# Optimization experiments

Hardware: AMD Instinct MI355X
Metric: run time of the kernel (lower is better)

## Reference

```python
import jax, jax.numpy as jnp
import numpy as np

SEQ_LEN = 32768
HID = 1024


def setup_inputs() -> dict:
    key = jax.random.key(0)
    k1, k2, k3, k4 = jax.random.split(key, 4)
    hidden = jax.random.normal(k1, (1, 1, HID), dtype=jnp.float32)
    encoder_outputs = jax.random.normal(k2, (SEQ_LEN, HID), dtype=jnp.float32)
    # nn.Linear(hidden_size, hidden_size): weight [H, H], bias [H]
    W = jax.random.normal(k3, (HID, HID), dtype=jnp.float32) * (1.0 / np.sqrt(HID))
    b = jax.random.normal(k4, (HID,), dtype=jnp.float32) * 0.01
    return {"hidden": hidden, "encoder_outputs": encoder_outputs, "W": W, "b": b}


def reference(hidden, encoder_outputs, W, b):
    # method == 'general':
    #   energy_i = Linear(enc_i) = W @ enc_i + b     -> [S, H]
    #   e_i = sum(hidden[-1, 0] * energy_i)           -> [S]
    h = hidden[-1, 0]                                 # [H]
    proj = jnp.einsum('sh,dh->sd', encoder_outputs, W) + b  # [S, H]
    energies = proj @ h                               # [S]
    attn = jax.nn.softmax(energies, axis=0)           # [S]
    return attn[None, None, :]                        # [1, 1, S]
```

## Files before the change

kernel.cpp:

```cpp
#include <hip/hip_runtime.h>
#include <hip/hip_bf16.h>
#include <math.h>

#define SEQ_LEN 32768
#define HID 1024

__global__ void __launch_bounds__(256) k_matvec(const float* __restrict__ W,
                                                const float* __restrict__ hvec,
                                                float* __restrict__ v) {
    __shared__ float red[256];
    const int t = threadIdx.x;
    const int col = (blockIdx.x << 5) + (t & 31);
    const int slice = t >> 5;
    const int d0 = slice << 7;
    float acc = 0.f;
#pragma unroll 8
    for (int dd = 0; dd < 128; ++dd) {
        const int d = d0 + dd;
        acc += hvec[d] * W[d * HID + col];
    }
    red[t] = acc;
    __syncthreads();
    if (t < 32) {
        float s = 0.f;
#pragma unroll
        for (int i = 0; i < 8; ++i) s += red[(i << 5) + t];
        v[(blockIdx.x << 5) + t] = s;
    }
}

__global__ void __launch_bounds__(256) k_energy(const float* __restrict__ enc,
                                                const float* __restrict__ v,
                                                float* __restrict__ energies,
                                                float2* __restrict__ bstats) {
    const int t = threadIdx.x;
    const int wave = t >> 6;
    const int lane = t & 63;
    const int row0 = (blockIdx.x << 5) + (wave << 3);

    const float4 vr0 = *reinterpret_cast<const float4*>(v +       (lane << 2));
    const float4 vr1 = *reinterpret_cast<const float4*>(v + 256 + (lane << 2));
    const float4 vr2 = *reinterpret_cast<const float4*>(v + 512 + (lane << 2));
    const float4 vr3 = *reinterpret_cast<const float4*>(v + 768 + (lane << 2));

    float m = -__builtin_inff();
    float z = 0.f;

#pragma unroll 2
    for (int r = 0; r < 8; ++r) {
        const size_t row = (size_t)(row0 + r);
        const float4* p = reinterpret_cast<const float4*>(enc + row * HID) + lane;
        const float4 a = p[0];
        const float4 b = p[64];
        const float4 c = p[128];
        const float4 d = p[192];
        float acc = a.x * vr0.x + a.y * vr0.y + a.z * vr0.z + a.w * vr0.w
                  + b.x * vr1.x + b.y * vr1.y + b.z * vr1.z + b.w * vr1.w
                  + c.x * vr2.x + c.y * vr2.y + c.z * vr2.z + c.w * vr2.w
                  + d.x * vr3.x + d.y * vr3.y + d.z * vr3.z + d.w * vr3.w;
#pragma unroll
        for (int off = 32; off; off >>= 1) acc += __shfl_xor(acc, off, 64);
        if (lane == 0) energies[row] = acc;
        const float nm = fmaxf(m, acc);
        z = z * __expf(m - nm) + __expf(acc - nm);
        m = nm;
    }

    __shared__ float wm[4], wz[4];
    if (lane == 0) { wm[wave] = m; wz[wave] = z; }
    __syncthreads();
    if (t == 0) {
        float M = fmaxf(fmaxf(wm[0], wm[1]), fmaxf(wm[2], wm[3]));
        float Z = wz[0] * __expf(wm[0] - M) + wz[1] * __expf(wm[1] - M)
                + wz[2] * __expf(wm[2] - M) + wz[3] * __expf(wm[3] - M);
        bstats[blockIdx.x] = make_float2(M, Z);
    }
}

__global__ void __launch_bounds__(256) k_final(const float* __restrict__ energies,
                                               const float2* __restrict__ bstats,
                                               float* __restrict__ out) {
    __shared__ float sm[256], sz[256];
    const int t = threadIdx.x;
    float m = -__builtin_inff();
    float z = 0.f;
#pragma unroll
    for (int i = 0; i < 4; ++i) {
        const float2 s = bstats[t + (i << 8)];
        const float nm = fmaxf(m, s.x);
        z = z * __expf(m - nm) + s.y * __expf(s.x - nm);
        m = nm;
    }
    sm[t] = m; sz[t] = z;
    __syncthreads();
    for (int off = 128; off; off >>= 1) {
        if (t < off) {
            const float m1 = sm[t], z1 = sz[t];
            const float m2 = sm[t + off], z2 = sz[t + off];
            const float M = fmaxf(m1, m2);
            sm[t] = M;
            sz[t] = z1 * __expf(m1 - M) + z2 * __expf(m2 - M);
        }
        __syncthreads();
    }
    const float M = sm[0];
    const float rZ = 1.f / sz[0];

    const size_t i = ((size_t)blockIdx.x << 9) + ((size_t)t << 1);
    const float2 e = *reinterpret_cast<const float2*>(energies + i);
    float2 o;
    o.x = __expf(e.x - M) * rZ;
    o.y = __expf(e.y - M) * rZ;
    *reinterpret_cast<float2*>(out + i) = o;
}

extern "C" void kernel_launch(void* const* d_in, const int* in_sizes, int n_in,
                              void* d_out, int out_size, void* d_ws, size_t ws_size,
                              hipStream_t stream) {
    const float* hidden = (const float*)d_in[0];
    const float* enc    = (const float*)d_in[1];
    const float* W      = (const float*)d_in[2];

    float* ws       = (float*)d_ws;
    float* v        = ws;
    float* energies = ws + HID;
    float2* bstats  = (float2*)(ws + HID + SEQ_LEN);

    k_matvec<<<HID / 32, 256, 0, stream>>>(W, hidden, v);
    k_energy<<<SEQ_LEN / 32, 256, 0, stream>>>(enc, v, energies, bstats);
    k_final<<<SEQ_LEN / 512, 256, 0, stream>>>(energies, bstats, (float*)d_out);
}
```

Baseline: 37.10 us.

## Spread matvec over one block per column and prefetch next encoder row

The W·h matvec now launches one block per output column instead of 32 blocks of 32 columns. Each thread strides over the hidden dimension, and the result is reduced with wave shuffles plus a small shared-memory step. This raises parallelism for the latency-bound first kernel, but W reads become strided across rows and rely on L2 to absorb the poor coalescing. The energy kernel is fully unrolled and register double-buffers the next row's float4 loads while computing the current dot product, to hide global-load latency.

```diff
diff --git a/kernel.cpp b/kernel.cpp
--- a/kernel.cpp
+++ b/kernel.cpp
@@ -8,25 +8,20 @@
 __global__ void __launch_bounds__(256) k_matvec(const float* __restrict__ W,
                                                 const float* __restrict__ hvec,
                                                 float* __restrict__ v) {
-    __shared__ float red[256];
+    const int col = blockIdx.x;
     const int t = threadIdx.x;
-    const int col = (blockIdx.x << 5) + (t & 31);
-    const int slice = t >> 5;
-    const int d0 = slice << 7;
     float acc = 0.f;
-#pragma unroll 8
-    for (int dd = 0; dd < 128; ++dd) {
-        const int d = d0 + dd;
-        acc += hvec[d] * W[d * HID + col];
+#pragma unroll
+    for (int i = 0; i < 4; ++i) {
+        const int d = (i << 8) + t;
+        acc = fmaf(hvec[d], W[d * HID + col], acc);
     }
-    red[t] = acc;
+#pragma unroll
+    for (int off = 32; off; off >>= 1) acc += __shfl_xor(acc, off, 64);
+    __shared__ float red[4];
+    if ((t & 63) == 0) red[t >> 6] = acc;
     __syncthreads();
-    if (t < 32) {
-        float s = 0.f;
-#pragma unroll
-        for (int i = 0; i < 8; ++i) s += red[(i << 5) + t];
-        v[(blockIdx.x << 5) + t] = s;
-    }
+    if (t == 0) v[col] = (red[0] + red[1]) + (red[2] + red[3]);
 }
 
 __global__ void __launch_bounds__(256) k_energy(const float* __restrict__ enc,
@@ -46,24 +41,27 @@
     float m = -__builtin_inff();
     float z = 0.f;
 
-#pragma unroll 2
+    const float4* p = reinterpret_cast<const float4*>(enc + (size_t)row0 * HID) + lane;
+    float4 a = p[0], b = p[64], c = p[128], d = p[192];
+
+#pragma unroll
     for (int r = 0; r < 8; ++r) {
-        const size_t row = (size_t)(row0 + r);
-        const float4* p = reinterpret_cast<const float4*>(enc + row * HID) + lane;
-        const float4 a = p[0];
-        const float4 b = p[64];
-        const float4 c = p[128];
-        const float4 d = p[192];
+        float4 na, nb, nc, nd;
+        if (r < 7) {
+            const float4* q = p + (size_t)(r + 1) * 256;
+            na = q[0]; nb = q[64]; nc = q[128]; nd = q[192];
+        }
         float acc = a.x * vr0.x + a.y * vr0.y + a.z * vr0.z + a.w * vr0.w
                   + b.x * vr1.x + b.y * vr1.y + b.z * vr1.z + b.w * vr1.w
                   + c.x * vr2.x + c.y * vr2.y + c.z * vr2.z + c.w * vr2.w
                   + d.x * vr3.x + d.y * vr3.y + d.z * vr3.z + d.w * vr3.w;
 #pragma unroll
         for (int off = 32; off; off >>= 1) acc += __shfl_xor(acc, off, 64);
-        if (lane == 0) energies[row] = acc;
+        if (lane == 0) energies[row0 + r] = acc;
         const float nm = fmaxf(m, acc);
         z = z * __expf(m - nm) + __expf(acc - nm);
         m = nm;
+        a = na; b = nb; c = nc; d = nd;
     }
 
     __shared__ float wm[4], wz[4];
@@ -126,7 +124,7 @@
     float* energies = ws + HID;
     float2* bstats  = (float2*)(ws + HID + SEQ_LEN);
 
-    k_matvec<<<HID / 32, 256, 0, stream>>>(W, hidden, v);
+    k_matvec<<<HID, 256, 0, stream>>>(W, hidden, v);
     k_energy<<<SEQ_LEN / 32, 256, 0, stream>>>(enc, v, energies, bstats);
     k_final<<<SEQ_LEN / 512, 256, 0, stream>>>(energies, bstats, (float*)d_out);
 }
```

New measurement: 37.00 us. About the same (-0.3%).
